# Kernel optimization log

Hardware: AMD Instinct MI355X
Metric: run time of the kernel (lower is better)

Reference implementation:

```python
import jax, jax.numpy as jnp
import numpy as np

H = 32


def setup_inputs() -> dict:
    key = jax.random.key(0)
    k_x, k_wih, k_whh, k_bih, k_bhh = jax.random.split(key, 5)
    B, T = 256, 2048
    scale = 1.0 / np.sqrt(H)  # matches torch LSTM uniform(-1/sqrt(H), 1/sqrt(H)) init scale
    x = jax.random.normal(k_x, (B, T, H), dtype=jnp.float32)
    W_ih = jax.random.uniform(k_wih, (4 * H, H), minval=-scale, maxval=scale, dtype=jnp.float32)
    W_hh = jax.random.uniform(k_whh, (4 * H, H), minval=-scale, maxval=scale, dtype=jnp.float32)
    b_ih = jax.random.uniform(k_bih, (4 * H,), minval=-scale, maxval=scale, dtype=jnp.float32)
    b_hh = jax.random.uniform(k_bhh, (4 * H,), minval=-scale, maxval=scale, dtype=jnp.float32)
    return {"x": x, "W_ih": W_ih, "W_hh": W_hh, "b_ih": b_ih, "b_hh": b_hh}


def reference(x, W_ih, W_hh, b_ih, b_hh):
    # Single-layer LSTM (PyTorch gate order: i, f, g, o), then clamp to [-1, 1].
    B, T, _ = x.shape
    # Precompute input projection for all timesteps in one big GEMM: [B, T, 4H]
    x_gates = jnp.einsum('bth,gh->btg', x, W_ih) + b_ih + b_hh

    def step(carry, xg_t):
        h, c = carry  # each [B, H]
        gates = xg_t + h @ W_hh.T  # [B, 4H]
        i, f, g, o = jnp.split(gates, 4, axis=-1)
        i = jax.nn.sigmoid(i)
        f = jax.nn.sigmoid(f)
        g = jnp.tanh(g)
        o = jax.nn.sigmoid(o)
        c = f * c + i * g
        h = o * jnp.tanh(c)
        return (h, c), h

    h0 = jnp.zeros((B, H), dtype=x.dtype)
    c0 = jnp.zeros((B, H), dtype=x.dtype)
    _, hs = jax.lax.scan(step, (h0, c0), jnp.swapaxes(x_gates, 0, 1))  # hs: [T, B, H]
    out = jnp.swapaxes(hs, 0, 1)  # [B, T, H]
    return jnp.clip(out, -1.0, 1.0)
```

## Files before the change

kernel.cpp:

```cpp
#include <hip/hip_runtime.h>

#define BB 256
#define TT 2048
#define HH 32
#define G4 128
#define POS 32

__device__ __forceinline__ float fsig(float x) {
    return __builtin_amdgcn_rcpf(1.0f + __expf(-x));
}
__device__ __forceinline__ float ftanh(float x) {
    return 1.0f - 2.0f * __builtin_amdgcn_rcpf(__expf(2.0f * x) + 1.0f);
}

__global__ __launch_bounds__(128) void xproj_kernel(
    const float* __restrict__ x, const float* __restrict__ W_ih,
    const float* __restrict__ b_ih, const float* __restrict__ b_hh,
    float* __restrict__ xg) {
  const int tid = threadIdx.x;
  const int g = tid & 3, j = tid >> 2;
  const int row = g * HH + j;

  float w[HH];
  const float4* wr = (const float4*)(W_ih + (size_t)row * HH);
#pragma unroll
  for (int k4 = 0; k4 < HH / 4; ++k4) {
    float4 v = wr[k4];
    w[k4 * 4 + 0] = v.x; w[k4 * 4 + 1] = v.y;
    w[k4 * 4 + 2] = v.z; w[k4 * 4 + 3] = v.w;
  }
  const float bias = b_ih[row] + b_hh[row];

  __shared__ float4 sx[POS * HH / 4];
  const size_t bt0 = (size_t)blockIdx.x * POS;
  const float4* xsrc = (const float4*)x + bt0 * (HH / 4);
  sx[tid] = xsrc[tid];
  sx[tid + 128] = xsrc[tid + 128];
  __syncthreads();

#pragma unroll 4
  for (int p = 0; p < POS; ++p) {
    const float4* xr = sx + p * (HH / 4);
    float a = bias;
#pragma unroll
    for (int k4 = 0; k4 < HH / 4; ++k4) {
      float4 v = xr[k4];
      a = fmaf(w[k4 * 4 + 0], v.x, a);
      a = fmaf(w[k4 * 4 + 1], v.y, a);
      a = fmaf(w[k4 * 4 + 2], v.z, a);
      a = fmaf(w[k4 * 4 + 3], v.w, a);
    }
    xg[(bt0 + p) * G4 + tid] = a;
  }
}

template <bool HAS_XG>
__global__ __launch_bounds__(64, 1) void lstm_rec(
    const float* __restrict__ x, const float* __restrict__ W_ih,
    const float* __restrict__ W_hh, const float* __restrict__ b_ih,
    const float* __restrict__ b_hh, const float4* __restrict__ xg,
    float* __restrict__ out) {
  const int b = blockIdx.x;
  const int lane = threadIdx.x;
  const int j = lane & 31;
  const int hf = lane >> 5;
  const int r0 = (hf * 2 + 0) * HH + j;
  const int r1 = (hf * 2 + 1) * HH + j;

  float whh0[HH], whh1[HH];
  {
    const float4* w0 = (const float4*)(W_hh + (size_t)r0 * HH);
    const float4* w1 = (const float4*)(W_hh + (size_t)r1 * HH);
#pragma unroll
    for (int k4 = 0; k4 < HH / 4; ++k4) {
      float4 a = w0[k4], c = w1[k4];
      whh0[k4 * 4 + 0] = a.x; whh0[k4 * 4 + 1] = a.y;
      whh0[k4 * 4 + 2] = a.z; whh0[k4 * 4 + 3] = a.w;
      whh1[k4 * 4 + 0] = c.x; whh1[k4 * 4 + 1] = c.y;
      whh1[k4 * 4 + 2] = c.z; whh1[k4 * 4 + 3] = c.w;
    }
  }

  float wih0[HH], wih1[HH];
  float bias0 = 0.f, bias1 = 0.f;
  if (!HAS_XG) {
    const float4* w0 = (const float4*)(W_ih + (size_t)r0 * HH);
    const float4* w1 = (const float4*)(W_ih + (size_t)r1 * HH);
#pragma unroll
    for (int k4 = 0; k4 < HH / 4; ++k4) {
      float4 a = w0[k4], c = w1[k4];
      wih0[k4 * 4 + 0] = a.x; wih0[k4 * 4 + 1] = a.y;
      wih0[k4 * 4 + 2] = a.z; wih0[k4 * 4 + 3] = a.w;
      wih1[k4 * 4 + 0] = c.x; wih1[k4 * 4 + 1] = c.y;
      wih1[k4 * 4 + 2] = c.z; wih1[k4 * 4 + 3] = c.w;
    }
    bias0 = b_ih[r0] + b_hh[r0];
    bias1 = b_ih[r1] + b_hh[r1];
  }

  float h = 0.f, c = 0.f;
  const size_t base = (size_t)b * TT;

  float4 xg_n = make_float4(0.f, 0.f, 0.f, 0.f);
  float xv_n = 0.f;
  if (HAS_XG) xg_n = xg[base * (G4 / 4) + j];
  else        xv_n = x[base * HH + j];

  for (int t = 0; t < TT; ++t) {
    float4 xgc = xg_n;
    float xvc = xv_n;
    {
      const int tn = (t + 1 < TT) ? t + 1 : TT - 1;
      if (HAS_XG) xg_n = xg[(base + tn) * (G4 / 4) + j];
      else        xv_n = x[(base + tn) * HH + j];
    }

    float hk[HH];
#pragma unroll
    for (int k = 0; k < HH; ++k)
      hk[k] = __uint_as_float(
          __builtin_amdgcn_readlane(__float_as_uint(h), k));

    float a0, a1;
    if (HAS_XG) {
      a0 = hf ? xgc.z : xgc.x;
      a1 = hf ? xgc.w : xgc.y;
    } else {
      a0 = bias0;
      a1 = bias1;
    }

    if (!HAS_XG) {
      float xk[HH];
#pragma unroll
      for (int k = 0; k < HH; ++k)
        xk[k] = __uint_as_float(
            __builtin_amdgcn_readlane(__float_as_uint(xvc), k));
#pragma unroll
      for (int k = 0; k < HH; ++k) {
        a0 = fmaf(wih0[k], xk[k], a0);
        a1 = fmaf(wih1[k], xk[k], a1);
      }
    }

#pragma unroll
    for (int k = 0; k < HH; ++k) {
      a0 = fmaf(whh0[k], hk[k], a0);
      a1 = fmaf(whh1[k], hk[k], a1);
    }

    const float o0 = __shfl_xor(a0, 32);
    const float o1 = __shfl_xor(a1, 32);
    const float ai = hf ? o0 : a0;
    const float af = hf ? o1 : a1;
    const float ag = hf ? a0 : o0;
    const float ao = hf ? a1 : o1;

    const float gi = fsig(ai);
    const float gf = fsig(af);
    const float gg = ftanh(ag);
    const float go = fsig(ao);
    c = fmaf(gf, c, gi * gg);
    h = go * ftanh(c);

    if (!hf)
      out[(base + t) * HH + j] = fminf(fmaxf(h, -1.f), 1.f);
  }
}

extern "C" void kernel_launch(void* const* d_in, const int* in_sizes, int n_in,
                              void* d_out, int out_size, void* d_ws,
                              size_t ws_size, hipStream_t stream) {
  const float* x    = (const float*)d_in[0];
  const float* W_ih = (const float*)d_in[1];
  const float* W_hh = (const float*)d_in[2];
  const float* b_ih = (const float*)d_in[3];
  const float* b_hh = (const float*)d_in[4];
  float* out = (float*)d_out;

  const size_t need = (size_t)BB * TT * G4 * sizeof(float);
  if (ws_size >= need) {
    float* xg = (float*)d_ws;
    xproj_kernel<<<BB * TT / POS, 128, 0, stream>>>(x, W_ih, b_ih, b_hh, xg);
    lstm_rec<true><<<BB, 64, 0, stream>>>(x, W_ih, W_hh, b_ih, b_hh,
                                          (const float4*)xg, out);
  } else {
    lstm_rec<false><<<BB, 64, 0, stream>>>(x, W_ih, W_hh, b_ih, b_hh, nullptr,
                                           out);
  }
}
```

Measured before the change: 1.076 ms.

## Restructure LSTM: gate-interleaved xproj layout, 4-step prefetch, split FMA chains

The input-projection kernel now writes gates interleaved per hidden unit as float4 (i,f,g,o), using a transposed W_ih in shared memory with 256 threads per block. The recurrent kernel unrolls time by 4 and prefetches the next four xg vectors, which hides global-load latency behind several dependent steps. It also splits each 32-term dot product into two independent FMA chains to shorten the serial critical path, and uses empty asm constraints to keep the weights pinned in registers. The risks are extra register pressure and a different summation order, which changes floating-point results slightly.

```diff
diff --git a/kernel.cpp b/kernel.cpp
--- a/kernel.cpp
+++ b/kernel.cpp
@@ -4,66 +4,90 @@
 #define TT 2048
 #define HH 32
 #define G4 128
-#define POS 32
+#define XB 32
 
 __device__ __forceinline__ float fsig(float x) {
-    return __builtin_amdgcn_rcpf(1.0f + __expf(-x));
+  return __builtin_amdgcn_rcpf(1.0f + __expf(-x));
 }
 __device__ __forceinline__ float ftanh(float x) {
-    return 1.0f - 2.0f * __builtin_amdgcn_rcpf(__expf(2.0f * x) + 1.0f);
-}
-
-__global__ __launch_bounds__(128) void xproj_kernel(
+  return 1.0f - 2.0f * __builtin_amdgcn_rcpf(__expf(2.0f * x) + 1.0f);
+}
+
+#define KEEP8(a)                                                          \
+  asm(""                                                                  \
+      : "+v"((a)[0]), "+v"((a)[1]), "+v"((a)[2]), "+v"((a)[3]),           \
+        "+v"((a)[4]), "+v"((a)[5]), "+v"((a)[6]), "+v"((a)[7]))
+
+__global__ __launch_bounds__(256) void xproj2(
     const float* __restrict__ x, const float* __restrict__ W_ih,
     const float* __restrict__ b_ih, const float* __restrict__ b_hh,
-    float* __restrict__ xg) {
+    float4* __restrict__ xg) {
+  __shared__ float wT[HH][G4 + 1];
+  __shared__ float xs[XB * HH];
+  __shared__ float bias[G4];
   const int tid = threadIdx.x;
-  const int g = tid & 3, j = tid >> 2;
-  const int row = g * HH + j;
-
-  float w[HH];
-  const float4* wr = (const float4*)(W_ih + (size_t)row * HH);
-#pragma unroll
-  for (int k4 = 0; k4 < HH / 4; ++k4) {
-    float4 v = wr[k4];
-    w[k4 * 4 + 0] = v.x; w[k4 * 4 + 1] = v.y;
-    w[k4 * 4 + 2] = v.z; w[k4 * 4 + 3] = v.w;
-  }
-  const float bias = b_ih[row] + b_hh[row];
-
-  __shared__ float4 sx[POS * HH / 4];
-  const size_t bt0 = (size_t)blockIdx.x * POS;
-  const float4* xsrc = (const float4*)x + bt0 * (HH / 4);
-  sx[tid] = xsrc[tid];
-  sx[tid + 128] = xsrc[tid + 128];
+
+#pragma unroll
+  for (int i = tid; i < G4 * HH; i += 256) wT[i & 31][i >> 5] = W_ih[i];
+  if (tid < G4) bias[tid] = b_ih[tid] + b_hh[tid];
+  const size_t bt0 = (size_t)blockIdx.x * XB;
+  ((float4*)xs)[tid] = ((const float4*)(x + bt0 * HH))[tid];
   __syncthreads();
 
-#pragma unroll 4
-  for (int p = 0; p < POS; ++p) {
-    const float4* xr = sx + p * (HH / 4);
-    float a = bias;
-#pragma unroll
-    for (int k4 = 0; k4 < HH / 4; ++k4) {
-      float4 v = xr[k4];
-      a = fmaf(w[k4 * 4 + 0], v.x, a);
-      a = fmaf(w[k4 * 4 + 1], v.y, a);
-      a = fmaf(w[k4 * 4 + 2], v.z, a);
-      a = fmaf(w[k4 * 4 + 3], v.w, a);
-    }
-    xg[(bt0 + p) * G4 + tid] = a;
-  }
-}
-
-template <bool HAS_XG>
-__global__ __launch_bounds__(64, 1) void lstm_rec(
-    const float* __restrict__ x, const float* __restrict__ W_ih,
-    const float* __restrict__ W_hh, const float* __restrict__ b_ih,
-    const float* __restrict__ b_hh, const float4* __restrict__ xg,
+  const int j = tid & 31, btl = tid >> 5;
+  const float b0 = bias[j], b1 = bias[HH + j], b2 = bias[2 * HH + j],
+              b3 = bias[3 * HH + j];
+#pragma unroll
+  for (int q = 0; q < 4; ++q) {
+    const int p = btl + 8 * q;
+    const float* xr = xs + p * HH;
+    float a0 = b0, a1 = b1, a2 = b2, a3 = b3;
+#pragma unroll
+    for (int k = 0; k < HH; ++k) {
+      const float xv = xr[k];
+      a0 = fmaf(wT[k][j], xv, a0);
+      a1 = fmaf(wT[k][HH + j], xv, a1);
+      a2 = fmaf(wT[k][2 * HH + j], xv, a2);
+      a3 = fmaf(wT[k][3 * HH + j], xv, a3);
+    }
+    xg[(bt0 + p) * HH + j] = make_float4(a0, a1, a2, a3);
+  }
+}
+
+#define STEP(xi, tt)                                                        \
+  {                                                                         \
+    float hk[HH];                                                           \
+    _Pragma("unroll") for (int k = 0; k < HH; ++k) hk[k] =                  \
+        __uint_as_float(__builtin_amdgcn_readlane(__float_as_uint(h), k));  \
+    float a0 = hf ? (xi).z : (xi).x;                                        \
+    float a1 = hf ? (xi).w : (xi).y;                                        \
+    float s0 = 0.f, s1 = 0.f;                                               \
+    _Pragma("unroll") for (int k = 0; k < 16; ++k) {                        \
+      a0 = fmaf(whh0[k], hk[k], a0);                                        \
+      a1 = fmaf(whh1[k], hk[k], a1);                                        \
+      s0 = fmaf(whh0[k + 16], hk[k + 16], s0);                              \
+      s1 = fmaf(whh1[k + 16], hk[k + 16], s1);                              \
+    }                                                                       \
+    a0 += s0;                                                               \
+    a1 += s1;                                                               \
+    const float o0 = __shfl_xor(a0, 32);                                    \
+    const float o1 = __shfl_xor(a1, 32);                                    \
+    const float ai = hf ? o0 : a0;                                          \
+    const float af = hf ? o1 : a1;                                          \
+    const float ag = hf ? a0 : o0;                                          \
+    const float ao = hf ? a1 : o1;                                          \
+    const float gi = fsig(ai), gf = fsig(af), go = fsig(ao);                \
+    const float gg = ftanh(ag);                                             \
+    c = fmaf(gf, c, gi * gg);                                               \
+    h = go * ftanh(c);                                                      \
+    if (!hf) outp[(tt)*HH + j] = fminf(fmaxf(h, -1.f), 1.f);                \
+  }
+
+__global__ __launch_bounds__(64, 1) void lstm_rec2(
+    const float4* __restrict__ xg, const float* __restrict__ W_hh,
     float* __restrict__ out) {
   const int b = blockIdx.x;
-  const int lane = threadIdx.x;
-  const int j = lane & 31;
-  const int hf = lane >> 5;
+  const int lane = threadIdx.x, j = lane & 31, hf = lane >> 5;
   const int r0 = (hf * 2 + 0) * HH + j;
   const int r1 = (hf * 2 + 1) * HH + j;
 
@@ -73,98 +97,106 @@
     const float4* w1 = (const float4*)(W_hh + (size_t)r1 * HH);
 #pragma unroll
     for (int k4 = 0; k4 < HH / 4; ++k4) {
-      float4 a = w0[k4], c = w1[k4];
+      float4 a = w0[k4], d = w1[k4];
       whh0[k4 * 4 + 0] = a.x; whh0[k4 * 4 + 1] = a.y;
       whh0[k4 * 4 + 2] = a.z; whh0[k4 * 4 + 3] = a.w;
-      whh1[k4 * 4 + 0] = c.x; whh1[k4 * 4 + 1] = c.y;
-      whh1[k4 * 4 + 2] = c.z; whh1[k4 * 4 + 3] = c.w;
-    }
-  }
-
-  float wih0[HH], wih1[HH];
-  float bias0 = 0.f, bias1 = 0.f;
-  if (!HAS_XG) {
-    const float4* w0 = (const float4*)(W_ih + (size_t)r0 * HH);
-    const float4* w1 = (const float4*)(W_ih + (size_t)r1 * HH);
-#pragma unroll
-    for (int k4 = 0; k4 < HH / 4; ++k4) {
-      float4 a = w0[k4], c = w1[k4];
-      wih0[k4 * 4 + 0] = a.x; wih0[k4 * 4 + 1] = a.y;
-      wih0[k4 * 4 + 2] = a.z; wih0[k4 * 4 + 3] = a.w;
-      wih1[k4 * 4 + 0] = c.x; wih1[k4 * 4 + 1] = c.y;
-      wih1[k4 * 4 + 2] = c.z; wih1[k4 * 4 + 3] = c.w;
-    }
-    bias0 = b_ih[r0] + b_hh[r0];
-    bias1 = b_ih[r1] + b_hh[r1];
+      whh1[k4 * 4 + 0] = d.x; whh1[k4 * 4 + 1] = d.y;
+      whh1[k4 * 4 + 2] = d.z; whh1[k4 * 4 + 3] = d.w;
+    }
   }
 
   float h = 0.f, c = 0.f;
   const size_t base = (size_t)b * TT;
-
-  float4 xg_n = make_float4(0.f, 0.f, 0.f, 0.f);
-  float xv_n = 0.f;
-  if (HAS_XG) xg_n = xg[base * (G4 / 4) + j];
-  else        xv_n = x[base * HH + j];
+  const float4* src = xg + base * HH + j;
+  float* outp = out + base * HH;
+
+  float4 c0 = src[0], c1 = src[HH], c2 = src[2 * HH], c3 = src[3 * HH];
+  for (int t = 0; t < TT; t += 4) {
+    KEEP8(whh0); KEEP8(whh0 + 8); KEEP8(whh0 + 16); KEEP8(whh0 + 24);
+    KEEP8(whh1); KEEP8(whh1 + 8); KEEP8(whh1 + 16); KEEP8(whh1 + 24);
+
+    const int tp = (t + 4 < TT) ? t + 4 : TT - 4;
+    float4 n0 = src[(size_t)(tp + 0) * HH];
+    float4 n1 = src[(size_t)(tp + 1) * HH];
+    float4 n2 = src[(size_t)(tp + 2) * HH];
+    float4 n3 = src[(size_t)(tp + 3) * HH];
+    STEP(c0, t);
+    STEP(c1, t + 1);
+    STEP(c2, t + 2);
+    STEP(c3, t + 3);
+    c0 = n0; c1 = n1; c2 = n2; c3 = n3;
+  }
+}
+
+__global__ __launch_bounds__(64, 1) void lstm_rec_fused(
+    const float* __restrict__ x, const float* __restrict__ W_ih,
+    const float* __restrict__ W_hh, const float* __restrict__ b_ih,
+    const float* __restrict__ b_hh, float* __restrict__ out) {
+  const int b = blockIdx.x;
+  const int lane = threadIdx.x, j = lane & 31, hf = lane >> 5;
+  const int r0 = (hf * 2 + 0) * HH + j;
+  const int r1 = (hf * 2 + 1) * HH + j;
+
+  float whh0[HH], whh1[HH], wih0[HH], wih1[HH];
+#pragma unroll
+  for (int k4 = 0; k4 < HH / 4; ++k4) {
+    float4 a = ((const float4*)(W_hh + (size_t)r0 * HH))[k4];
+    float4 d = ((const float4*)(W_hh + (size_t)r1 * HH))[k4];
+    float4 e = ((const float4*)(W_ih + (size_t)r0 * HH))[k4];
+    float4 f = ((const float4*)(W_ih + (size_t)r1 * HH))[k4];
+    whh0[k4 * 4 + 0] = a.x; whh0[k4 * 4 + 1] = a.y;
+    whh0[k4 * 4 + 2] = a.z; whh0[k4 * 4 + 3] = a.w;
+    whh1[k4 * 4 + 0] = d.x; whh1[k4 * 4 + 1] = d.y;
+    whh1[k4 * 4 + 2] = d.z; whh1[k4 * 4 + 3] = d.w;
+    wih0[k4 * 4 + 0] = e.x; wih0[k4 * 4 + 1] = e.y;
+    wih0[k4 * 4 + 2] = e.z; wih0[k4 * 4 + 3] = e.w;
+    wih1[k4 * 4 + 0] = f.x; wih1[k4 * 4 + 1] = f.y;
+    wih1[k4 * 4 + 2] = f.z; wih1[k4 * 4 + 3] = f.w;
+  }
+  const float bias0 = b_ih[r0] + b_hh[r0];
+  const float bias1 = b_ih[r1] + b_hh[r1];
+
+  float h = 0.f, c = 0.f;
+  const size_t base = (size_t)b * TT;
+  float* outp = out + base * HH;
+  float xv_n = x[base * HH + j];
 
   for (int t = 0; t < TT; ++t) {
-    float4 xgc = xg_n;
-    float xvc = xv_n;
-    {
-      const int tn = (t + 1 < TT) ? t + 1 : TT - 1;
-      if (HAS_XG) xg_n = xg[(base + tn) * (G4 / 4) + j];
-      else        xv_n = x[(base + tn) * HH + j];
-    }
-
-    float hk[HH];
-#pragma unroll
-    for (int k = 0; k < HH; ++k)
-      hk[k] = __uint_as_float(
-          __builtin_amdgcn_readlane(__float_as_uint(h), k));
-
-    float a0, a1;
-    if (HAS_XG) {
-      a0 = hf ? xgc.z : xgc.x;
-      a1 = hf ? xgc.w : xgc.y;
-    } else {
-      a0 = bias0;
-      a1 = bias1;
-    }
-
-    if (!HAS_XG) {
-      float xk[HH];
-#pragma unroll
-      for (int k = 0; k < HH; ++k)
-        xk[k] = __uint_as_float(
-            __builtin_amdgcn_readlane(__float_as_uint(xvc), k));
-#pragma unroll
-      for (int k = 0; k < HH; ++k) {
-        a0 = fmaf(wih0[k], xk[k], a0);
-        a1 = fmaf(wih1[k], xk[k], a1);
-      }
-    }
-
+    KEEP8(whh0); KEEP8(whh0 + 8); KEEP8(whh0 + 16); KEEP8(whh0 + 24);
+    KEEP8(whh1); KEEP8(whh1 + 8); KEEP8(whh1 + 16); KEEP8(whh1 + 24);
+    KEEP8(wih0); KEEP8(wih0 + 8); KEEP8(wih0 + 16); KEEP8(wih0 + 24);
+    KEEP8(wih1); KEEP8(wih1 + 8); KEEP8(wih1 + 16); KEEP8(wih1 + 24);
+
+    const float xvc = xv_n;
+    const int tn = (t + 1 < TT) ? t + 1 : TT - 1;
+    xv_n = x[(base + tn) * HH + j];
+
+    float hk[HH], xk[HH];
 #pragma unroll
     for (int k = 0; k < HH; ++k) {
+      hk[k] = __uint_as_float(__builtin_amdgcn_readlane(__float_as_uint(h), k));
+      xk[k] =
+          __uint_as_float(__builtin_amdgcn_readlane(__float_as_uint(xvc), k));
+    }
+    float a0 = bias0, a1 = bias1;
+#pragma unroll
+    for (int k = 0; k < HH; ++k) {
+      a0 = fmaf(wih0[k], xk[k], a0);
+      a1 = fmaf(wih1[k], xk[k], a1);
       a0 = fmaf(whh0[k], hk[k], a0);
       a1 = fmaf(whh1[k], hk[k], a1);
     }
-
     const float o0 = __shfl_xor(a0, 32);
     const float o1 = __shfl_xor(a1, 32);
     const float ai = hf ? o0 : a0;
     const float af = hf ? o1 : a1;
     const float ag = hf ? a0 : o0;
     const float ao = hf ? a1 : o1;
-
-    const float gi = fsig(ai);
-    const float gf = fsig(af);
+    const float gi = fsig(ai), gf = fsig(af), go = fsig(ao);
     const float gg = ftanh(ag);
-    const float go = fsig(ao);
     c = fmaf(gf, c, gi * gg);
     h = go * ftanh(c);
-
-    if (!hf)
-      out[(base + t) * HH + j] = fminf(fmaxf(h, -1.f), 1.f);
+    if (!hf) outp[t * HH + j] = fminf(fmaxf(h, -1.f), 1.f);
   }
 }
 
@@ -180,12 +212,10 @@
 
   const size_t need = (size_t)BB * TT * G4 * sizeof(float);
   if (ws_size >= need) {
-    float* xg = (float*)d_ws;
-    xproj_kernel<<<BB * TT / POS, 128, 0, stream>>>(x, W_ih, b_ih, b_hh, xg);
-    lstm_rec<true><<<BB, 64, 0, stream>>>(x, W_ih, W_hh, b_ih, b_hh,
-                                          (const float4*)xg, out);
+    float4* xg = (float4*)d_ws;
+    xproj2<<<BB * TT / XB, 256, 0, stream>>>(x, W_ih, b_ih, b_hh, xg);
+    lstm_rec2<<<BB, 64, 0, stream>>>(xg, W_hh, out);
   } else {
-    lstm_rec<false><<<BB, 64, 0, stream>>>(x, W_ih, W_hh, b_ih, b_hh, nullptr,
-                                           out);
-  }
-}
+    lstm_rec_fused<<<BB, 64, 0, stream>>>(x, W_ih, W_hh, b_ih, b_hh, out);
+  }
+}
```

New measurement: 1.096 ms. Within noise of the previous version (+1.8%).
